# Optimization experiments

Measured on AMD Instinct MI355X. Metric: run time of the kernel, lower is better.

Reference implementation:

```python
import jax, jax.numpy as jnp
import numpy as np

N = 50000      # nodes
E = 800000     # edges (avg degree 16)
IN = 128       # in_channels
OUT = 64       # out_channels
HID = 2 * OUT  # 128, hidden width of conv1
EPS = 1e-5     # BatchNorm eps


def _edge_norm(edge_index):
    # PyG ChebConv with sym normalization, lambda_max=2: L_hat = -D^{-1/2} A D^{-1/2}
    src, dst = edge_index[0], edge_index[1]
    deg = jax.ops.segment_sum(jnp.ones((E,), jnp.float32), src, num_segments=N)
    dinv = jnp.where(deg > 0, jax.lax.rsqrt(jnp.maximum(deg, 1.0)), 0.0)
    return -dinv[src] * dinv[dst]


def _cheb(x, src, dst, norm, W0, W1, b):
    # K=2 Chebyshev conv: Tx0 = x, Tx1 = L_hat x (sparse propagate)
    tx1 = jax.ops.segment_sum(x[src] * norm[:, None], dst, num_segments=N)
    return x @ W0 + tx1 @ W1 + b


def setup_inputs() -> dict:
    key = jax.random.key(0)
    ks = jax.random.split(key, 14)
    g = lambda k, shp, fan: jax.random.normal(k, shp, jnp.float32) / np.sqrt(fan)
    return {
        "x": jax.random.normal(ks[0], (N, IN), jnp.float32),
        "edge_index": jax.random.randint(ks[1], (2, E), 0, N, dtype=jnp.int32),
        "W1_0": g(ks[2], (IN, HID), IN),
        "W1_1": g(ks[3], (IN, HID), IN),
        "b1": jnp.zeros((HID,), jnp.float32),
        "gamma": jnp.ones((HID,), jnp.float32),
        "beta": jnp.zeros((HID,), jnp.float32),
        "Wmu_0": g(ks[4], (HID, OUT), HID),
        "Wmu_1": g(ks[5], (HID, OUT), HID),
        "b_mu": jnp.zeros((OUT,), jnp.float32),
        "Wls_0": g(ks[6], (HID, OUT), HID),
        "Wls_1": g(ks[7], (HID, OUT), HID),
        "b_ls": jnp.zeros((OUT,), jnp.float32),
    }


def reference(x, edge_index, W1_0, W1_1, b1, gamma, beta,
              Wmu_0, Wmu_1, b_mu, Wls_0, Wls_1, b_ls):
    src, dst = edge_index[0], edge_index[1]
    norm = _edge_norm(edge_index)
    h = _cheb(x, src, dst, norm, W1_0, W1_1, b1)         # [N, HID]
    # BatchNorm1d (training mode: batch statistics over nodes)
    mean = jnp.mean(h, axis=0)
    var = jnp.var(h, axis=0)
    h = (h - mean) * jax.lax.rsqrt(var + EPS) * gamma + beta
    h = jax.nn.relu(h)
    mu = _cheb(h, src, dst, norm, Wmu_0, Wmu_1, b_mu)    # [N, OUT]
    logstd = _cheb(h, src, dst, norm, Wls_0, Wls_1, b_ls)
    return (mu, logstd)
```

## Files before the change

### kernel.cpp

```cpp
#include <hip/hip_runtime.h>
#include <cstddef>
#include <cstdint>

static constexpr int IN_C  = 128;
static constexpr float BN_EPS = 1e-5f;
static constexpr int OUT_C = 64;

static constexpr int CS_C = 32;
static constexpr int CS_R = 8;
static constexpr int CS_RANGE = 6250;

using bf16x8 = __attribute__((ext_vector_type(8))) short;
using f32x4  = __attribute__((ext_vector_type(4))) float;

__device__ __forceinline__ ushort f2bf(float f) {
    uint u = __float_as_uint(f);
    u += 0x7fffu + ((u >> 16) & 1u);
    return (ushort)(u >> 16);
}
__device__ __forceinline__ uint pack2(float a, float b) {
    return (uint)f2bf(a) | ((uint)f2bf(b) << 16);
}
__device__ __forceinline__ float bf_lo(uint v) { return __uint_as_float(v << 16); }
__device__ __forceinline__ float bf_hi(uint v) { return __uint_as_float(v & 0xffff0000u); }

__global__ __launch_bounds__(1024) void hist_k(
    const int* __restrict__ src, const int* __restrict__ dst,
    int* __restrict__ hsrc_part, int* __restrict__ hdst_part,
    int N, int E, int chunk, int range) {
    __shared__ int hs_[CS_RANGE];
    __shared__ int hd_[CS_RANGE];
    int c = blockIdx.x & (CS_C - 1);
    int r = blockIdx.x / CS_C;
    int base = r * range;
    int hi = min(base + range, N);
    int rsz = hi - base;
    for (int j = threadIdx.x; j < rsz; j += 1024) { hs_[j] = 0; hd_[j] = 0; }
    __syncthreads();
    int e0 = c * chunk, e1 = min(e0 + chunk, E);
    for (int i = e0 + threadIdx.x; i < e1; i += 1024) {
        int s = src[i];
        if (s >= base && s < hi) atomicAdd(&hs_[s - base], 1);
        int t = dst[i];
        if (t >= base && t < hi) atomicAdd(&hd_[t - base], 1);
    }
    __syncthreads();
    for (int j = threadIdx.x; j < rsz; j += 1024) {
        hsrc_part[(size_t)c * N + base + j] = hs_[j];
        hdst_part[(size_t)c * N + base + j] = hd_[j];
    }
}

__global__ __launch_bounds__(1024) void count_k(
    const int* __restrict__ hsrc_part, const int* __restrict__ hdst_part,
    float* __restrict__ dinv, int* __restrict__ cnt_dst,
    int* __restrict__ bsum, float* __restrict__ stats, int N) {
    __shared__ int sw[16];
    int tid = threadIdx.x;
    if (blockIdx.x == 0 && tid < 256) stats[tid] = 0.f;
    int base = blockIdx.x * 4096;
    int tsum = 0;
    #pragma unroll
    for (int j = 0; j < 4; ++j) {
        int v = base + j * 1024 + tid;
        if (v < N) {
            int a = 0, b = 0;
            for (int c = 0; c < CS_C; ++c) {
                a += hsrc_part[(size_t)c * N + v];
                b += hdst_part[(size_t)c * N + v];
            }
            dinv[v] = (a > 0) ? rsqrtf((float)a) : 0.f;
            cnt_dst[v] = b;
            tsum += b;
        }
    }
    #pragma unroll
    for (int off = 1; off < 64; off <<= 1) tsum += __shfl_xor(tsum, off, 64);
    if ((tid & 63) == 0) sw[tid >> 6] = tsum;
    __syncthreads();
    if (tid == 0) {
        int a = 0;
        #pragma unroll
        for (int w = 0; w < 16; ++w) a += sw[w];
        bsum[blockIdx.x] = a;
    }
}

__global__ __launch_bounds__(1024) void phase3_k(
    const int* __restrict__ cnt, const int* __restrict__ bsum,
    int* __restrict__ row_ptr, int* __restrict__ hdst_part, int n, int nb) {
    __shared__ int sm_w[16];
    __shared__ int sm_excl[16];
    __shared__ int sm_base;
    int tid = threadIdx.x;
    int lane = tid & 63, wid = tid >> 6;
    int base = blockIdx.x * 4096;
    if (tid == 0) {
        int run = 0;
        for (int b = 0; b < (int)blockIdx.x; ++b) run += bsum[b];
        sm_base = run;
        if (blockIdx.x == 0) row_ptr[0] = 0;
    }
    int i0 = base + tid * 4;
    int c0 = (i0     < n) ? cnt[i0]     : 0;
    int c1 = (i0 + 1 < n) ? cnt[i0 + 1] : 0;
    int c2 = (i0 + 2 < n) ? cnt[i0 + 2] : 0;
    int c3 = (i0 + 3 < n) ? cnt[i0 + 3] : 0;
    int tsum = c0 + c1 + c2 + c3;
    int s = tsum;
    #pragma unroll
    for (int off = 1; off < 64; off <<= 1) {
        int t = __shfl_up(s, off, 64);
        if (lane >= off) s += t;
    }
    if (lane == 63) sm_w[wid] = s;
    __syncthreads();
    if (tid == 0) {
        int acc = 0;
        #pragma unroll
        for (int w = 0; w < 16; ++w) { sm_excl[w] = acc; acc += sm_w[w]; }
    }
    __syncthreads();
    int excl = sm_base + sm_excl[wid] + (s - tsum);
    int st0 = excl, st1 = excl + c0, st2 = st1 + c1, st3 = st2 + c2;
    if (i0     < n) row_ptr[i0 + 1] = st1;
    if (i0 + 1 < n) row_ptr[i0 + 2] = st2;
    if (i0 + 2 < n) row_ptr[i0 + 3] = st3;
    if (i0 + 3 < n) row_ptr[i0 + 4] = excl + tsum;
    int r0 = st0, r1 = st1, r2 = st2, r3 = st3;
    for (int c = 0; c < CS_C; ++c) {
        size_t idx = (size_t)c * n + i0;
        if (i0 + 3 < n) {
            int4 t = *(const int4*)(hdst_part + idx);
            int4 o = make_int4(r0, r1, r2, r3);
            *(int4*)(hdst_part + idx) = o;
            r0 += t.x; r1 += t.y; r2 += t.z; r3 += t.w;
        } else {
            if (i0 < n)     { int t = hdst_part[idx];     hdst_part[idx] = r0;     r0 += t; }
            if (i0 + 1 < n) { int t = hdst_part[idx + 1]; hdst_part[idx + 1] = r1; r1 += t; }
            if (i0 + 2 < n) { int t = hdst_part[idx + 2]; hdst_part[idx + 2] = r2; r2 += t; }
        }
    }
}

__global__ __launch_bounds__(1024) void scatter_k(
    const int* __restrict__ src, const int* __restrict__ dst,
    const int* __restrict__ off, int* __restrict__ col,
    int N, int E, int chunk, int range) {
    __shared__ int cur[CS_RANGE];
    int c = blockIdx.x & (CS_C - 1);
    int r = blockIdx.x / CS_C;
    int base = r * range;
    int hi = min(base + range, N);
    int rsz = hi - base;
    for (int j = threadIdx.x; j < rsz; j += 1024)
        cur[j] = off[(size_t)c * N + base + j];
    __syncthreads();
    int e0 = c * chunk, e1 = min(e0 + chunk, E);
    for (int i = e0 + threadIdx.x; i < e1; i += 1024) {
        int t = dst[i];
        if (t >= base && t < hi) {
            int pos = atomicAdd(&cur[t - base], 1);
            col[pos] = src[i];
        }
    }
}

__global__ void convert_prep_k(const float* __restrict__ in, const float* __restrict__ dinv,
                               ushort* __restrict__ xb, ushort* __restrict__ xsb, int n64,
                               int nb_conv,
                               const float* __restrict__ W1_0, const float* __restrict__ W1_1,
                               const float* __restrict__ b1,
                               const float* __restrict__ Wmu_0, const float* __restrict__ Wmu_1,
                               const float* __restrict__ b_mu,
                               const float* __restrict__ Wls_0, const float* __restrict__ Wls_1,
                               const float* __restrict__ b_ls,
                               ushort* __restrict__ Wt1, ushort* __restrict__ Wt2,
                               float* __restrict__ bias1, float* __restrict__ bias2) {
    int bid = blockIdx.x;
    if (bid < nb_conv) {
        int i = bid * 256 + threadIdx.x;
        if (i >= n64) return;
        int row = i >> 6;
        float d = dinv[row];
        float2 v = ((const float2*)in)[i];
        ((uint*)xb)[i] = pack2(v.x, v.y);
        ((uint*)xsb)[i] = pack2(v.x * d, v.y * d);
    } else {
        int idx = (bid - nb_conv) * 256 + threadIdx.x;
        int which = idx >> 15;
        int c = (idx >> 8) & 127;
        int k = idx & 255;
        if (which == 0) {
            float v = (k < 128) ? W1_0[k * 128 + c] : W1_1[(k - 128) * 128 + c];
            Wt1[c * 256 + k] = f2bf(v);
            if (k == 0) bias1[c] = b1[c];
        } else {
            float v;
            if (c < 64) v = (k < 128) ? Wmu_0[k * 64 + c] : Wmu_1[(k - 128) * 64 + c];
            else        v = (k < 128) ? Wls_0[k * 64 + (c - 64)] : Wls_1[(k - 128) * 64 + (c - 64)];
            Wt2[c * 256 + k] = f2bf(v);
            if (k == 0) bias2[c] = (c < 64) ? b_mu[c] : b_ls[c - 64];
        }
    }
}

#define ACC8(V)                                         \
    acc[0] += bf_lo((V).x); acc[1] += bf_hi((V).x);     \
    acc[2] += bf_lo((V).y); acc[3] += bf_hi((V).y);     \
    acc[4] += bf_lo((V).z); acc[5] += bf_hi((V).z);     \
    acc[6] += bf_lo((V).w); acc[7] += bf_hi((V).w);

__global__ __launch_bounds__(256) void propagate4_k(
    const uint4* __restrict__ xs, uint4* __restrict__ out,
    const int* __restrict__ row_ptr, const int* __restrict__ col,
    const float* __restrict__ dinv, int n) {
    int wid = (blockIdx.x * 256 + threadIdx.x) >> 6;
    if (wid >= n) return;
    int lane = threadIdx.x & 63;
    int g = lane >> 4, li = lane & 15;
    int s = row_ptr[wid], e = row_ptr[wid + 1];
    float acc[8];
    #pragma unroll
    for (int k = 0; k < 8; ++k) acc[k] = 0.f;
    int i = s + g;
    for (; i + 12 < e; i += 16) {
        int c0 = col[i];
        int c1 = col[i + 4];
        int c2 = col[i + 8];
        int c3 = col[i + 12];
        uint4 v0 = xs[(size_t)c0 * 16 + li];
        uint4 v1 = xs[(size_t)c1 * 16 + li];
        uint4 v2 = xs[(size_t)c2 * 16 + li];
        uint4 v3 = xs[(size_t)c3 * 16 + li];
        ACC8(v0); ACC8(v1); ACC8(v2); ACC8(v3);
    }
    for (; i < e; i += 4) {
        int c0 = col[i];
        uint4 v0 = xs[(size_t)c0 * 16 + li];
        ACC8(v0);
    }
    #pragma unroll
    for (int k = 0; k < 8; ++k) {
        acc[k] += __shfl_xor(acc[k], 16, 64);
        acc[k] += __shfl_xor(acc[k], 32, 64);
    }
    if (g == 0) {
        float sc = -dinv[wid];
        uint4 o;
        o.x = pack2(acc[0] * sc, acc[1] * sc);
        o.y = pack2(acc[2] * sc, acc[3] * sc);
        o.z = pack2(acc[4] * sc, acc[5] * sc);
        o.w = pack2(acc[6] * sc, acc[7] * sc);
        out[(size_t)wid * 16 + li] = o;
    }
}

template <int MODE>
__global__ __launch_bounds__(256) void gemm_mfma_k(
    const ushort* __restrict__ A0, const ushort* __restrict__ A1,
    const ushort* __restrict__ Wt, const float* __restrict__ bias,
    ushort* __restrict__ Cb, float* __restrict__ Cmu, float* __restrict__ Cls, int n) {
    __shared__ ushort sA[64][32];
    __shared__ ushort sW[128][32];

    int tid = threadIdx.x;
    int block_row = blockIdx.x * 64;
    int wave = tid >> 6, lane = tid & 63;
    int m_local = wave * 16 + (lane & 15);
    int quad = lane >> 4;

    f32x4 acc[8];
    #pragma unroll
    for (int t = 0; t < 8; ++t) acc[t] = (f32x4){0.f, 0.f, 0.f, 0.f};

    for (int k0 = 0; k0 < 256; k0 += 32) {
        {
            int row = tid >> 2, koff = (tid & 3) * 8;
            int grow = block_row + row;
            int kc = k0 + koff;
            uint4 v = make_uint4(0, 0, 0, 0);
            if (grow < n) {
                const ushort* srcp = (kc < 128) ? (A0 + (size_t)grow * 128 + kc)
                                                : (A1 + (size_t)grow * 128 + (kc - 128));
                v = *(const uint4*)srcp;
            }
            *(uint4*)&sA[row][koff] = v;
        }
        #pragma unroll
        for (int i = tid; i < 512; i += 256) {
            int c = i >> 2, koff = (i & 3) * 8;
            *(uint4*)&sW[c][koff] = *(const uint4*)(Wt + (size_t)c * 256 + k0 + koff);
        }
        __syncthreads();
        bf16x8 af = *(const bf16x8*)&sA[m_local][quad * 8];
        #pragma unroll
        for (int t = 0; t < 8; ++t) {
            bf16x8 bfr = *(const bf16x8*)&sW[t * 16 + (lane & 15)][quad * 8];
            acc[t] = __builtin_amdgcn_mfma_f32_16x16x32_bf16(af, bfr, acc[t], 0, 0, 0);
        }
        __syncthreads();
    }

    int col_base = lane & 15;
    int row_l = wave * 16 + quad * 4;
    #pragma unroll
    for (int t = 0; t < 8; ++t) {
        int col = t * 16 + col_base;
        float b = bias[col];
        #pragma unroll
        for (int r = 0; r < 4; ++r) {
            int grow = block_row + row_l + r;
            if (grow < n) {
                float v = acc[t][r] + b;
                if (MODE == 0) {
                    Cb[(size_t)grow * 128 + col] = f2bf(v);
                } else {
                    if (col < 64) Cmu[(size_t)grow * 64 + col] = v;
                    else          Cls[(size_t)grow * 64 + (col - 64)] = v;
                }
            }
        }
    }
}

__global__ __launch_bounds__(256) void bn_stats_k(const ushort* __restrict__ hb,
                                                  float* __restrict__ stats, int n) {
    __shared__ float sm[1024];
    int tid = threadIdx.x;
    int p = tid & 63;
    int rw = tid >> 6;
    float s0 = 0.f, q0 = 0.f, s1 = 0.f, q1 = 0.f;
    for (int r = blockIdx.x * 4 + rw; r < n; r += gridDim.x * 4) {
        uint v = ((const uint*)hb)[(size_t)r * 64 + p];
        float f0 = bf_lo(v), f1 = bf_hi(v);
        s0 += f0; q0 += f0 * f0;
        s1 += f1; q1 += f1 * f1;
    }
    sm[tid] = s0; sm[256 + tid] = q0; sm[512 + tid] = s1; sm[768 + tid] = q1;
    __syncthreads();
    if (tid < 64) {
        #pragma unroll
        for (int q = 0; q < 4; ++q) {
            float v = sm[q * 256 + tid] + sm[q * 256 + tid + 64] +
                      sm[q * 256 + tid + 128] + sm[q * 256 + tid + 192];
            int col = 2 * tid + (q >> 1);
            atomicAdd(&stats[col + ((q & 1) ? 128 : 0)], v);
        }
    }
}

__global__ __launch_bounds__(256) void bn_apply_k(
    ushort* __restrict__ hb, ushort* __restrict__ hsb,
    const float* __restrict__ stats, const float* __restrict__ gamma,
    const float* __restrict__ beta, const float* __restrict__ dinv,
    float inv_n, int n64) {
    __shared__ float sp[256];
    int tid = threadIdx.x;
    if (tid < 128) {
        float mean = stats[tid] * inv_n;
        float var = stats[128 + tid] * inv_n - mean * mean;
        float sc = gamma[tid] * rsqrtf(var + BN_EPS);
        sp[tid] = sc;
        sp[128 + tid] = beta[tid] - mean * sc;
    }
    __syncthreads();
    int i = blockIdx.x * 256 + tid;
    if (i >= n64) return;
    int c2 = (i & 63) * 2;
    int row = i >> 6;
    uint v = ((uint*)hb)[i];
    float f0 = fmaxf(bf_lo(v) * sp[c2]     + sp[128 + c2],     0.f);
    float f1 = fmaxf(bf_hi(v) * sp[c2 + 1] + sp[128 + c2 + 1], 0.f);
    ((uint*)hb)[i] = pack2(f0, f1);
    float d = dinv[row];
    ((uint*)hsb)[i] = pack2(f0 * d, f1 * d);
}

extern "C" void kernel_launch(void* const* d_in, const int* in_sizes, int n_in,
                              void* d_out, int out_size, void* d_ws, size_t ws_size,
                              hipStream_t stream) {
    const float* x = (const float*)d_in[0];
    const int* edge_index = (const int*)d_in[1];
    const float* W1_0 = (const float*)d_in[2];
    const float* W1_1 = (const float*)d_in[3];
    const float* b1 = (const float*)d_in[4];
    const float* gamma = (const float*)d_in[5];
    const float* beta = (const float*)d_in[6];
    const float* Wmu_0 = (const float*)d_in[7];
    const float* Wmu_1 = (const float*)d_in[8];
    const float* b_mu = (const float*)d_in[9];
    const float* Wls_0 = (const float*)d_in[10];
    const float* Wls_1 = (const float*)d_in[11];
    const float* b_ls = (const float*)d_in[12];

    const int N = in_sizes[0] / IN_C;
    const int E = in_sizes[1] / 2;
    const int* src = edge_index;
    const int* dst = edge_index + E;

    char* w = (char*)d_ws;
    auto alloc = [&](size_t bytes) {
        char* p = w;
        w += (bytes + 15) & ~(size_t)15;
        return p;
    };
    float* stats = (float*)alloc(256 * 4);
    int* row_ptr = (int*)alloc((size_t)(N + 1) * 4);
    int* bsum    = (int*)alloc(64 * 4);
    float* dinv  = (float*)alloc((size_t)N * 4);
    int* cnt_dst = (int*)alloc((size_t)N * 4);
    int* col     = (int*)alloc((size_t)E * 4);
    int* hsrc_part = (int*)alloc((size_t)CS_C * N * 4);
    int* hdst_part = (int*)alloc((size_t)CS_C * N * 4);
    ushort* x_bf  = (ushort*)alloc((size_t)N * 128 * 2);
    ushort* xs_bf = (ushort*)alloc((size_t)N * 128 * 2);
    ushort* xp_bf = (ushort*)alloc((size_t)N * 128 * 2);
    ushort* h_bf  = (ushort*)alloc((size_t)N * 128 * 2);
    ushort* Wt1   = (ushort*)alloc(128 * 256 * 2);
    ushort* Wt2   = (ushort*)alloc(128 * 256 * 2);
    float* bias1  = (float*)alloc(128 * 4);
    float* bias2  = (float*)alloc(128 * 4);

    ushort* hs_bf = xs_bf;
    ushort* hp_bf = xp_bf;

    float* out_mu = (float*)d_out;
    float* out_ls = out_mu + (size_t)N * OUT_C;

    int chunk = (E + CS_C - 1) / CS_C;
    int range = (N + CS_R - 1) / CS_R;
    int NB = (N + 4095) / 4096;
    int nb_conv = (N * 64 + 255) / 256;

    hist_k<<<CS_R * CS_C, 1024, 0, stream>>>(src, dst, hsrc_part, hdst_part, N, E, chunk, range);
    count_k<<<NB, 1024, 0, stream>>>(hsrc_part, hdst_part, dinv, cnt_dst, bsum, stats, N);
    phase3_k<<<NB, 1024, 0, stream>>>(cnt_dst, bsum, row_ptr, hdst_part, N, NB);
    scatter_k<<<CS_R * CS_C, 1024, 0, stream>>>(src, dst, hdst_part, col, N, E, chunk, range);

    convert_prep_k<<<nb_conv + 256, 256, 0, stream>>>(
        x, dinv, x_bf, xs_bf, N * 64, nb_conv,
        W1_0, W1_1, b1, Wmu_0, Wmu_1, b_mu, Wls_0, Wls_1, b_ls,
        Wt1, Wt2, bias1, bias2);

    int pb = (N + 3) / 4;
    propagate4_k<<<pb, 256, 0, stream>>>((const uint4*)xs_bf, (uint4*)xp_bf,
                                         row_ptr, col, dinv, N);

    int gb = (N + 63) / 64;
    gemm_mfma_k<0><<<gb, 256, 0, stream>>>(x_bf, xp_bf, Wt1, bias1, h_bf, nullptr, nullptr, N);

    bn_stats_k<<<256, 256, 0, stream>>>(h_bf, stats, N);
    bn_apply_k<<<(N * 64 + 255) / 256, 256, 0, stream>>>(h_bf, hs_bf, stats, gamma, beta,
                                                         dinv, 1.f / (float)N, N * 64);

    propagate4_k<<<pb, 256, 0, stream>>>((const uint4*)hs_bf, (uint4*)hp_bf,
                                         row_ptr, col, dinv, N);

    gemm_mfma_k<1><<<gb, 256, 0, stream>>>(h_bf, hp_bf, Wt2, bias2, nullptr, out_mu, out_ls, N);
}
```

Before: 313.0 us.

## Fuse BN statistics into GEMM epilogue, swizzle LDS, and parallelize CSR scan

Folds the BatchNorm sum and sum-of-squares reduction into the first MFMA GEMM epilogue, using wave shuffles, LDS and one atomic per column per block, so the separate bn_stats pass over h is removed. XOR-swizzles the LDS layouts of the A and W tiles to reduce bank conflicts on the MFMA operand reads. Rebuilds the degree/row_ptr prefix scan with 256-thread blocks plus a separate block-sum scan kernel, replacing the serial per-block prefix loop and giving more parallelism across N. Statistics now come from fp32 values before bf16 rounding, which changes numerics slightly, and there is one extra small launch.

```diff
diff --git a/kernel.cpp b/kernel.cpp
--- a/kernel.cpp
+++ b/kernel.cpp
@@ -23,6 +23,8 @@
 }
 __device__ __forceinline__ float bf_lo(uint v) { return __uint_as_float(v << 16); }
 __device__ __forceinline__ float bf_hi(uint v) { return __uint_as_float(v & 0xffff0000u); }
+
+__device__ __forceinline__ int swz8(int row, int g) { return (g ^ ((row >> 1) & 3)) * 8; }
 
 __global__ __launch_bounds__(1024) void hist_k(
     const int* __restrict__ src, const int* __restrict__ dst,
@@ -51,94 +53,76 @@
     }
 }
 
-__global__ __launch_bounds__(1024) void count_k(
+__global__ __launch_bounds__(256) void count_k(
     const int* __restrict__ hsrc_part, const int* __restrict__ hdst_part,
     float* __restrict__ dinv, int* __restrict__ cnt_dst,
     int* __restrict__ bsum, float* __restrict__ stats, int N) {
-    __shared__ int sw[16];
+    __shared__ int sw[4];
     int tid = threadIdx.x;
-    if (blockIdx.x == 0 && tid < 256) stats[tid] = 0.f;
-    int base = blockIdx.x * 4096;
-    int tsum = 0;
-    #pragma unroll
-    for (int j = 0; j < 4; ++j) {
-        int v = base + j * 1024 + tid;
-        if (v < N) {
-            int a = 0, b = 0;
-            for (int c = 0; c < CS_C; ++c) {
-                a += hsrc_part[(size_t)c * N + v];
-                b += hdst_part[(size_t)c * N + v];
-            }
-            dinv[v] = (a > 0) ? rsqrtf((float)a) : 0.f;
-            cnt_dst[v] = b;
-            tsum += b;
-        }
-    }
-    #pragma unroll
-    for (int off = 1; off < 64; off <<= 1) tsum += __shfl_xor(tsum, off, 64);
-    if ((tid & 63) == 0) sw[tid >> 6] = tsum;
-    __syncthreads();
-    if (tid == 0) {
+    if (blockIdx.x == 0) stats[tid] = 0.f;
+    int v = blockIdx.x * 256 + tid;
+    int b = 0;
+    if (v < N) {
         int a = 0;
-        #pragma unroll
-        for (int w = 0; w < 16; ++w) a += sw[w];
-        bsum[blockIdx.x] = a;
-    }
-}
-
-__global__ __launch_bounds__(1024) void phase3_k(
+        for (int c = 0; c < CS_C; ++c) {
+            a += hsrc_part[(size_t)c * N + v];
+            b += hdst_part[(size_t)c * N + v];
+        }
+        dinv[v] = (a > 0) ? rsqrtf((float)a) : 0.f;
+        cnt_dst[v] = b;
+    }
+    int t = b;
+    #pragma unroll
+    for (int off = 1; off < 64; off <<= 1) t += __shfl_xor(t, off, 64);
+    if ((tid & 63) == 0) sw[tid >> 6] = t;
+    __syncthreads();
+    if (tid == 0) bsum[blockIdx.x] = sw[0] + sw[1] + sw[2] + sw[3];
+}
+
+__global__ __launch_bounds__(256) void bscan_k(int* __restrict__ bsum, int nb) {
+    __shared__ int sm[256];
+    int tid = threadIdx.x;
+    int v = (tid < nb) ? bsum[tid] : 0;
+    sm[tid] = v;
+    __syncthreads();
+    #pragma unroll
+    for (int off = 1; off < 256; off <<= 1) {
+        int t = (tid >= off) ? sm[tid - off] : 0;
+        __syncthreads();
+        sm[tid] += t;
+        __syncthreads();
+    }
+    if (tid < nb) bsum[tid] = sm[tid] - v;
+}
+
+__global__ __launch_bounds__(256) void phase3_k(
     const int* __restrict__ cnt, const int* __restrict__ bsum,
-    int* __restrict__ row_ptr, int* __restrict__ hdst_part, int n, int nb) {
-    __shared__ int sm_w[16];
-    __shared__ int sm_excl[16];
-    __shared__ int sm_base;
+    int* __restrict__ row_ptr, int* __restrict__ hdst_part, int n) {
+    __shared__ int swv[4];
     int tid = threadIdx.x;
-    int lane = tid & 63, wid = tid >> 6;
-    int base = blockIdx.x * 4096;
-    if (tid == 0) {
-        int run = 0;
-        for (int b = 0; b < (int)blockIdx.x; ++b) run += bsum[b];
-        sm_base = run;
-        if (blockIdx.x == 0) row_ptr[0] = 0;
-    }
-    int i0 = base + tid * 4;
-    int c0 = (i0     < n) ? cnt[i0]     : 0;
-    int c1 = (i0 + 1 < n) ? cnt[i0 + 1] : 0;
-    int c2 = (i0 + 2 < n) ? cnt[i0 + 2] : 0;
-    int c3 = (i0 + 3 < n) ? cnt[i0 + 3] : 0;
-    int tsum = c0 + c1 + c2 + c3;
-    int s = tsum;
+    int lane = tid & 63, wave = tid >> 6;
+    int v = blockIdx.x * 256 + tid;
+    int c = (v < n) ? cnt[v] : 0;
+    int s = c;
     #pragma unroll
     for (int off = 1; off < 64; off <<= 1) {
         int t = __shfl_up(s, off, 64);
         if (lane >= off) s += t;
     }
-    if (lane == 63) sm_w[wid] = s;
-    __syncthreads();
-    if (tid == 0) {
-        int acc = 0;
-        #pragma unroll
-        for (int w = 0; w < 16; ++w) { sm_excl[w] = acc; acc += sm_w[w]; }
-    }
-    __syncthreads();
-    int excl = sm_base + sm_excl[wid] + (s - tsum);
-    int st0 = excl, st1 = excl + c0, st2 = st1 + c1, st3 = st2 + c2;
-    if (i0     < n) row_ptr[i0 + 1] = st1;
-    if (i0 + 1 < n) row_ptr[i0 + 2] = st2;
-    if (i0 + 2 < n) row_ptr[i0 + 3] = st3;
-    if (i0 + 3 < n) row_ptr[i0 + 4] = excl + tsum;
-    int r0 = st0, r1 = st1, r2 = st2, r3 = st3;
-    for (int c = 0; c < CS_C; ++c) {
-        size_t idx = (size_t)c * n + i0;
-        if (i0 + 3 < n) {
-            int4 t = *(const int4*)(hdst_part + idx);
-            int4 o = make_int4(r0, r1, r2, r3);
-            *(int4*)(hdst_part + idx) = o;
-            r0 += t.x; r1 += t.y; r2 += t.z; r3 += t.w;
-        } else {
-            if (i0 < n)     { int t = hdst_part[idx];     hdst_part[idx] = r0;     r0 += t; }
-            if (i0 + 1 < n) { int t = hdst_part[idx + 1]; hdst_part[idx + 1] = r1; r1 += t; }
-            if (i0 + 2 < n) { int t = hdst_part[idx + 2]; hdst_part[idx + 2] = r2; r2 += t; }
+    if (lane == 63) swv[wave] = s;
+    __syncthreads();
+    int wexcl = 0;
+    for (int w = 0; w < wave; ++w) wexcl += swv[w];
+    int st = bsum[blockIdx.x] + wexcl + (s - c);
+    if (v < n) row_ptr[v + 1] = st + c;
+    if (v == 0) row_ptr[0] = 0;
+    int r = st;
+    for (int ch = 0; ch < CS_C; ++ch) {
+        size_t idx = (size_t)ch * n + v;
+        if (v < n) {
+            int t = hdst_part[idx];
+            hdst_part[idx] = r;
+            r += t;
         }
     }
 }
@@ -260,15 +244,19 @@
 __global__ __launch_bounds__(256) void gemm_mfma_k(
     const ushort* __restrict__ A0, const ushort* __restrict__ A1,
     const ushort* __restrict__ Wt, const float* __restrict__ bias,
-    ushort* __restrict__ Cb, float* __restrict__ Cmu, float* __restrict__ Cls, int n) {
+    ushort* __restrict__ Cb, float* __restrict__ Cmu, float* __restrict__ Cls,
+    float* __restrict__ stats, int n) {
     __shared__ ushort sA[64][32];
     __shared__ ushort sW[128][32];
+    __shared__ float smS[4][128];
+    __shared__ float smQ[4][128];
 
     int tid = threadIdx.x;
     int block_row = blockIdx.x * 64;
     int wave = tid >> 6, lane = tid & 63;
-    int m_local = wave * 16 + (lane & 15);
+    int col_base = lane & 15;
     int quad = lane >> 4;
+    int m_local = wave * 16 + col_base;
 
     f32x4 acc[8];
     #pragma unroll
@@ -276,38 +264,39 @@
 
     for (int k0 = 0; k0 < 256; k0 += 32) {
         {
-            int row = tid >> 2, koff = (tid & 3) * 8;
+            int row = tid >> 2, g = tid & 3;
             int grow = block_row + row;
-            int kc = k0 + koff;
+            int kc = k0 + g * 8;
             uint4 v = make_uint4(0, 0, 0, 0);
             if (grow < n) {
                 const ushort* srcp = (kc < 128) ? (A0 + (size_t)grow * 128 + kc)
                                                 : (A1 + (size_t)grow * 128 + (kc - 128));
                 v = *(const uint4*)srcp;
             }
-            *(uint4*)&sA[row][koff] = v;
+            *(uint4*)&sA[row][swz8(row, g)] = v;
         }
         #pragma unroll
         for (int i = tid; i < 512; i += 256) {
-            int c = i >> 2, koff = (i & 3) * 8;
-            *(uint4*)&sW[c][koff] = *(const uint4*)(Wt + (size_t)c * 256 + k0 + koff);
+            int c = i >> 2, g = i & 3;
+            *(uint4*)&sW[c][swz8(c, g)] = *(const uint4*)(Wt + (size_t)c * 256 + k0 + g * 8);
         }
         __syncthreads();
-        bf16x8 af = *(const bf16x8*)&sA[m_local][quad * 8];
+        bf16x8 af = *(const bf16x8*)&sA[m_local][swz8(m_local, quad)];
         #pragma unroll
         for (int t = 0; t < 8; ++t) {
-            bf16x8 bfr = *(const bf16x8*)&sW[t * 16 + (lane & 15)][quad * 8];
+            int wr = t * 16 + col_base;
+            bf16x8 bfr = *(const bf16x8*)&sW[wr][swz8(wr, quad)];
             acc[t] = __builtin_amdgcn_mfma_f32_16x16x32_bf16(af, bfr, acc[t], 0, 0, 0);
         }
         __syncthreads();
     }
 
-    int col_base = lane & 15;
     int row_l = wave * 16 + quad * 4;
     #pragma unroll
     for (int t = 0; t < 8; ++t) {
         int col = t * 16 + col_base;
         float b = bias[col];
+        float s = 0.f, q = 0.f;
         #pragma unroll
         for (int r = 0; r < 4; ++r) {
             int grow = block_row + row_l + r;
@@ -315,37 +304,26 @@
                 float v = acc[t][r] + b;
                 if (MODE == 0) {
                     Cb[(size_t)grow * 128 + col] = f2bf(v);
+                    s += v; q += v * v;
                 } else {
                     if (col < 64) Cmu[(size_t)grow * 64 + col] = v;
                     else          Cls[(size_t)grow * 64 + (col - 64)] = v;
                 }
             }
         }
-    }
-}
-
-__global__ __launch_bounds__(256) void bn_stats_k(const ushort* __restrict__ hb,
-                                                  float* __restrict__ stats, int n) {
-    __shared__ float sm[1024];
-    int tid = threadIdx.x;
-    int p = tid & 63;
-    int rw = tid >> 6;
-    float s0 = 0.f, q0 = 0.f, s1 = 0.f, q1 = 0.f;
-    for (int r = blockIdx.x * 4 + rw; r < n; r += gridDim.x * 4) {
-        uint v = ((const uint*)hb)[(size_t)r * 64 + p];
-        float f0 = bf_lo(v), f1 = bf_hi(v);
-        s0 += f0; q0 += f0 * f0;
-        s1 += f1; q1 += f1 * f1;
-    }
-    sm[tid] = s0; sm[256 + tid] = q0; sm[512 + tid] = s1; sm[768 + tid] = q1;
-    __syncthreads();
-    if (tid < 64) {
-        #pragma unroll
-        for (int q = 0; q < 4; ++q) {
-            float v = sm[q * 256 + tid] + sm[q * 256 + tid + 64] +
-                      sm[q * 256 + tid + 128] + sm[q * 256 + tid + 192];
-            int col = 2 * tid + (q >> 1);
-            atomicAdd(&stats[col + ((q & 1) ? 128 : 0)], v);
+        if (MODE == 0) {
+            s += __shfl_xor(s, 16, 64); s += __shfl_xor(s, 32, 64);
+            q += __shfl_xor(q, 16, 64); q += __shfl_xor(q, 32, 64);
+            if (quad == 0) { smS[wave][col] = s; smQ[wave][col] = q; }
+        }
+    }
+    if (MODE == 0) {
+        __syncthreads();
+        if (tid < 128) {
+            float s = smS[0][tid] + smS[1][tid] + smS[2][tid] + smS[3][tid];
+            float q = smQ[0][tid] + smQ[1][tid] + smQ[2][tid] + smQ[3][tid];
+            atomicAdd(&stats[tid], s);
+            atomicAdd(&stats[128 + tid], q);
         }
     }
 }
@@ -407,7 +385,7 @@
     };
     float* stats = (float*)alloc(256 * 4);
     int* row_ptr = (int*)alloc((size_t)(N + 1) * 4);
-    int* bsum    = (int*)alloc(64 * 4);
+    int* bsum    = (int*)alloc(256 * 4);
     float* dinv  = (float*)alloc((size_t)N * 4);
     int* cnt_dst = (int*)alloc((size_t)N * 4);
     int* col     = (int*)alloc((size_t)E * 4);
@@ -430,12 +408,13 @@
 
     int chunk = (E + CS_C - 1) / CS_C;
     int range = (N + CS_R - 1) / CS_R;
-    int NB = (N + 4095) / 4096;
+    int NBLK = (N + 255) / 256;
     int nb_conv = (N * 64 + 255) / 256;
 
     hist_k<<<CS_R * CS_C, 1024, 0, stream>>>(src, dst, hsrc_part, hdst_part, N, E, chunk, range);
-    count_k<<<NB, 1024, 0, stream>>>(hsrc_part, hdst_part, dinv, cnt_dst, bsum, stats, N);
-    phase3_k<<<NB, 1024, 0, stream>>>(cnt_dst, bsum, row_ptr, hdst_part, N, NB);
+    count_k<<<NBLK, 256, 0, stream>>>(hsrc_part, hdst_part, dinv, cnt_dst, bsum, stats, N);
+    bscan_k<<<1, 256, 0, stream>>>(bsum, NBLK);
+    phase3_k<<<NBLK, 256, 0, stream>>>(cnt_dst, bsum, row_ptr, hdst_part, N);
     scatter_k<<<CS_R * CS_C, 1024, 0, stream>>>(src, dst, hdst_part, col, N, E, chunk, range);
 
     convert_prep_k<<<nb_conv + 256, 256, 0, stream>>>(
@@ -448,14 +427,15 @@
                                          row_ptr, col, dinv, N);
 
     int gb = (N + 63) / 64;
-    gemm_mfma_k<0><<<gb, 256, 0, stream>>>(x_bf, xp_bf, Wt1, bias1, h_bf, nullptr, nullptr, N);
-
-    bn_stats_k<<<256, 256, 0, stream>>>(h_bf, stats, N);
+    gemm_mfma_k<0><<<gb, 256, 0, stream>>>(x_bf, xp_bf, Wt1, bias1, h_bf,
+                                           nullptr, nullptr, stats, N);
+
     bn_apply_k<<<(N * 64 + 255) / 256, 256, 0, stream>>>(h_bf, hs_bf, stats, gamma, beta,
                                                          dinv, 1.f / (float)N, N * 64);
 
     propagate4_k<<<pb, 256, 0, stream>>>((const uint4*)hs_bf, (uint4*)hp_bf,
                                          row_ptr, col, dinv, N);
 
-    gemm_mfma_k<1><<<gb, 256, 0, stream>>>(h_bf, hp_bf, Wt2, bias2, nullptr, out_mu, out_ls, N);
-}
+    gemm_mfma_k<1><<<gb, 256, 0, stream>>>(h_bf, hp_bf, Wt2, bias2, nullptr,
+                                           out_mu, out_ls, stats, N);
+}
```

Result: faster. 291.2 us (-7.0%).
